# Kernel optimization log

Hardware: AMD Instinct MI355X
Metric: run time of the kernel (lower is better)

Reference implementation:

```python
import jax, jax.numpy as jnp
import numpy as np

BN_EPS = 1e-5

def _conv(x, w, pad):
    return jax.lax.conv_general_dilated(
        x, w, window_strides=(1, 1), padding=[(pad, pad), (pad, pad)],
        dimension_numbers=('NCHW', 'OIHW', 'NCHW'))

def setup_inputs() -> dict:
    key = jax.random.key(0)
    ks = jax.random.split(key, 6)
    B, C1, C2, H, W, k = 4, 128, 256, 64, 64, 3
    N = k * k
    x = jax.random.normal(ks[0], (B, C1, H, W), jnp.float32)
    pw_w = jax.random.normal(ks[1], (C2, C1, 1, 1), jnp.float32) * 0.05
    bn_gamma = jnp.ones((C2,), jnp.float32)
    bn_beta = jnp.zeros((C2,), jnp.float32)
    bn_mean = jax.random.normal(ks[2], (C2,), jnp.float32) * 0.1
    bn_var = jax.random.uniform(ks[3], (C2,), jnp.float32, minval=0.5, maxval=1.5)
    off_w = jax.random.normal(ks[4], (2 * N, C2, 3, 3), jnp.float32) * 0.01
    off_b = jnp.zeros((2 * N,), jnp.float32)
    dcn_w = jax.random.normal(ks[5], (C2, C2, k, k), jnp.float32) * 0.02
    return dict(x=x, pw_w=pw_w, bn_gamma=bn_gamma, bn_beta=bn_beta,
                bn_mean=bn_mean, bn_var=bn_var, off_w=off_w, off_b=off_b,
                dcn_w=dcn_w)

def reference(x, pw_w, bn_gamma, bn_beta, bn_mean, bn_var, off_w, off_b, dcn_w):
    B, C1, H, W = x.shape
    C2 = pw_w.shape[0]
    k = dcn_w.shape[-1]
    N = k * k
    # ---- 1x1 pointwise conv + BatchNorm (eval mode), act=False ----
    xp = _conv(x, pw_w, 0)
    scale = bn_gamma * jax.lax.rsqrt(bn_var + BN_EPS)
    xp = xp * scale[None, :, None, None] + (bn_beta - bn_mean * scale)[None, :, None, None]
    # ---- offset prediction conv: [B, 2N, H, W]; first N = dy, last N = dx ----
    offset = _conv(xp, off_w, 1) + off_b[None, :, None, None]
    off_y, off_x = offset[:, :N], offset[:, N:]
    # ---- sampling positions p = p0 + p_n + offset ----
    gy, gx = jnp.meshgrid(jnp.arange(H, dtype=jnp.float32),
                          jnp.arange(W, dtype=jnp.float32), indexing='ij')
    kk = jnp.arange(k, dtype=jnp.float32) - (k // 2)
    ky, kx = jnp.meshgrid(kk, kk, indexing='ij')
    py = gy[None, None] + ky.reshape(N)[None, :, None, None] + off_y  # [B,N,H,W]
    px = gx[None, None] + kx.reshape(N)[None, :, None, None] + off_x
    py = jnp.clip(py, 0.0, H - 1.0)
    px = jnp.clip(px, 0.0, W - 1.0)

    def sample_one(img, py_b, px_b):  # img [C2,H,W], py/px [N,H,W]
        y0 = jnp.floor(py_b)
        x0 = jnp.floor(px_b)
        wy = py_b - y0
        wx = px_b - x0
        y0i = y0.astype(jnp.int32)
        x0i = x0.astype(jnp.int32)
        y1i = jnp.minimum(y0i + 1, H - 1)
        x1i = jnp.minimum(x0i + 1, W - 1)
        flat = img.reshape(C2, H * W)
        def g(yy, xx):
            idx = (yy * W + xx).reshape(-1)
            return flat[:, idx].reshape(C2, N, H, W)
        v00 = g(y0i, x0i); v01 = g(y0i, x1i)
        v10 = g(y1i, x0i); v11 = g(y1i, x1i)
        wy = wy[None]; wx = wx[None]
        return (v00 * (1 - wy) * (1 - wx) + v01 * (1 - wy) * wx +
                v10 * wy * (1 - wx) + v11 * wy * wx)

    sampled = jax.vmap(sample_one)(xp, py, px)  # [B,C2,N,H,W]
    # ---- deformable conv = weighted sum over kernel points ----
    out = jnp.einsum('bcnhw,ocn->bohw', sampled, dcn_w.reshape(C2, C2, N))
    return jax.nn.silu(out)
```

## Files before the change

kernel.cpp:

```cpp
#include <hip/hip_runtime.h>
#include <math.h>

#define XP_F   0
#define OFF_F  4194304
#define XPH_F  4489216
#define WTB_F  6586368
#define PART_F 6881280
#define SAMP_F 9240576
#define SPLIT_END_F 28114944ULL

typedef short bf16x8 __attribute__((ext_vector_type(8)));
typedef float f32x4 __attribute__((ext_vector_type(4)));

__device__ inline unsigned short f2b(float f) {
    union { float f; unsigned u; } v; v.f = f;
    unsigned r = v.u + 0x7FFF + ((v.u >> 16) & 1);
    return (unsigned short)(r >> 16);
}
__device__ inline float b2f(unsigned short h) {
    union { unsigned u; float f; } v; v.u = ((unsigned)h) << 16; return v.f;
}

__global__ __launch_bounds__(256) void k0_prep(const float* __restrict__ dcn,
                                               unsigned short* __restrict__ wTb) {
    int idx = blockIdx.x * 256 + threadIdx.x;
    int n = idx >> 16, o = (idx >> 8) & 255, c = idx & 255;
    wTb[idx] = f2b(dcn[(o * 256 + c) * 9 + n]);
}

__global__ __launch_bounds__(256, 4) void k1_pw_bn(const float* __restrict__ x,
                                                   const float* __restrict__ pw,
                                                   const float* __restrict__ gamma,
                                                   const float* __restrict__ beta,
                                                   const float* __restrict__ mean,
                                                   const float* __restrict__ var,
                                                   float* __restrict__ xp,
                                                   unsigned short* __restrict__ xph) {
    __shared__ float wl[128 * 64];
    int t = threadIdx.x;
    int m0 = blockIdx.x * 64;
    int b = m0 >> 12;
    int hw = (m0 & 4095) + (t & 63);
    int q = t >> 6;
    int c2base = blockIdx.y * 64;

    for (int i = 0; i < 32; ++i) {
        int idx = t + 256 * i;
        int kk = idx >> 6, c2l = idx & 63;
        wl[idx] = pw[(c2base + c2l) * 128 + kk];
    }
    __syncthreads();

    float acc[16];
#pragma unroll
    for (int i = 0; i < 16; ++i) acc[i] = 0.f;

    const float* xb = x + (b * 128) * 4096 + hw;
    for (int kk = 0; kk < 128; kk += 8) {
        float xv[8];
#pragma unroll
        for (int u = 0; u < 8; ++u) xv[u] = xb[(kk + u) * 4096];
#pragma unroll
        for (int u = 0; u < 8; ++u) {
            const float4* w4 = (const float4*)&wl[(kk + u) * 64 + q * 16];
#pragma unroll
            for (int i = 0; i < 4; ++i) {
                float4 wv = w4[i];
                acc[i * 4 + 0] += xv[u] * wv.x;
                acc[i * 4 + 1] += xv[u] * wv.y;
                acc[i * 4 + 2] += xv[u] * wv.z;
                acc[i * 4 + 3] += xv[u] * wv.w;
            }
        }
    }
    bf16x8 r0, r1;
#pragma unroll
    for (int i = 0; i < 16; ++i) {
        int c2 = c2base + q * 16 + i;
        float s = gamma[c2] * rsqrtf(var[c2] + 1e-5f);
        float v = acc[i] * s + (beta[c2] - mean[c2] * s);
        xp[((b * 256 + c2) << 12) + hw] = v;
        if (i < 8) r0[i] = (short)f2b(v); else r1[i - 8] = (short)f2b(v);
    }
    unsigned short* hb = xph + (((b << 12) + hw) << 8) + c2base + q * 16;
    *(bf16x8*)hb = r0;
    *(bf16x8*)(hb + 8) = r1;
}

__global__ __launch_bounds__(256) void k2a_off(const float* __restrict__ xp,
                                               const float* __restrict__ offw,
                                               float* __restrict__ part) {
    __shared__ float xl[3 * 32 * 66];
    __shared__ float wl[9 * 18 * 32];
    int t = threadIdx.x;
    int bx = blockIdx.x;
    int b = bx >> 9, h = (bx >> 3) & 63, cs = bx & 7;
    int w = t & 63, jset = t >> 6;
    const int jbase_a[4] = {0, 5, 10, 14};
    const int jcnt_a[4] = {5, 5, 4, 4};
    int jbase = jbase_a[jset], jcnt = jcnt_a[jset];
    float acc[5] = {0.f, 0.f, 0.f, 0.f, 0.f};
    int cbase = cs * 32;

    for (int idx = t; idx < 3 * 32 * 66; idx += 256) {
        int dy = idx / 2112, rem = idx % 2112;
        int c = rem / 66, col = rem % 66;
        int y = h + dy - 1, wc = col - 1;
        float v = 0.f;
        if ((unsigned)y < 64u && (unsigned)wc < 64u)
            v = xp[((b * 256 + cbase + c) << 12) + y * 64 + wc];
        xl[idx] = v;
    }
    for (int idx = t; idx < 18 * 32 * 9; idx += 256) {
        int j = idx / 288, c = (idx / 9) % 32, tap = idx % 9;
        wl[(tap * 18 + j) * 32 + c] = offw[(j * 256 + cbase + c) * 9 + tap];
    }
    __syncthreads();
#pragma unroll
    for (int tap = 0; tap < 9; ++tap) {
        int dy = tap / 3, dx = tap % 3;
        const float* xrow = &xl[dy * 2112 + (w + dx)];
        const float4* wrow = (const float4*)&wl[(tap * 18 + jbase) * 32];
#pragma unroll
        for (int c4 = 0; c4 < 8; ++c4) {
            float xv0 = xrow[(c4 * 4 + 0) * 66];
            float xv1 = xrow[(c4 * 4 + 1) * 66];
            float xv2 = xrow[(c4 * 4 + 2) * 66];
            float xv3 = xrow[(c4 * 4 + 3) * 66];
#pragma unroll
            for (int jj = 0; jj < 5; ++jj) {
                if (jj < jcnt) {
                    float4 wv = wrow[jj * 8 + c4];
                    acc[jj] += xv0 * wv.x + xv1 * wv.y + xv2 * wv.z + xv3 * wv.w;
                }
            }
        }
    }
    for (int jj = 0; jj < 5; ++jj) {
        if (jj < jcnt)
            part[(((cs * 4 + b) * 18 + jbase + jj) << 12) + h * 64 + w] = acc[jj];
    }
}

__global__ __launch_bounds__(256) void k2b_red(const float* __restrict__ part,
                                               const float* __restrict__ offb,
                                               float* __restrict__ off) {
    int i = blockIdx.x * 256 + threadIdx.x;
    int j = (i >> 12) % 18;
    float s = offb[j];
#pragma unroll
    for (int cs = 0; cs < 8; ++cs) s += part[cs * 294912 + i];
    off[i] = s;
}

__global__ __launch_bounds__(256) void k3a_samp(const unsigned short* __restrict__ xph,
                                                const float* __restrict__ off,
                                                unsigned short* __restrict__ samp) {
    __shared__ int   c00[32], c01[32], c10[32], c11[32];
    __shared__ float4 wts[32];
    int t = threadIdx.x;
    int bid = blockIdx.x;
    int b = bid / 1152, r = bid % 1152;
    int tap = r >> 7, pb = r & 127;
    int h = pb >> 1, wh = (pb & 1) * 32;

    if (t < 32) {
        int w = wh + t;
        int hw = h * 64 + w;
        float oy = off[((b * 18 + tap) << 12) + hw];
        float ox = off[((b * 18 + tap + 9) << 12) + hw];
        float py = (float)(h + tap / 3 - 1) + oy;
        float px = (float)(w + tap % 3 - 1) + ox;
        py = fminf(fmaxf(py, 0.f), 63.f);
        px = fminf(fmaxf(px, 0.f), 63.f);
        float fy = floorf(py), fx = floorf(px);
        int y0 = (int)fy, x0 = (int)fx;
        float wy = py - fy, wx = px - fx;
        int y1 = min(y0 + 1, 63), x1 = min(x0 + 1, 63);
        c00[t] = (y0 * 64 + x0) << 8;  c01[t] = (y0 * 64 + x1) << 8;
        c10[t] = (y1 * 64 + x0) << 8;  c11[t] = (y1 * 64 + x1) << 8;
        wts[t] = make_float4((1.f - wy) * (1.f - wx), (1.f - wy) * wx,
                             wy * (1.f - wx), wy * wx);
    }
    __syncthreads();

    const unsigned short* xb = xph + (b << 20);
    unsigned short* sb = samp + bid * 8192;
#pragma unroll
    for (int i = 0; i < 4; ++i) {
        int u = i * 256 + t;
        int F = u >> 6, chunk = u & 63;
        int lane = chunk ^ (F & 7);
        int pxl = (F >> 3) * 16 + (lane & 15);
        int co = ((F & 7) * 4 + (lane >> 4)) << 3;
        float4 wv = wts[pxl];
        bf16x8 v00 = *(const bf16x8*)(xb + c00[pxl] + co);
        bf16x8 v01 = *(const bf16x8*)(xb + c01[pxl] + co);
        bf16x8 v10 = *(const bf16x8*)(xb + c10[pxl] + co);
        bf16x8 v11 = *(const bf16x8*)(xb + c11[pxl] + co);
        bf16x8 rr;
#pragma unroll
        for (int j = 0; j < 8; ++j) {
            float v = wv.x * b2f((unsigned short)v00[j]) +
                      wv.y * b2f((unsigned short)v01[j]) +
                      wv.z * b2f((unsigned short)v10[j]) +
                      wv.w * b2f((unsigned short)v11[j]);
            rr[j] = (short)f2b(v);
        }
        *(bf16x8*)(sb + (u << 3)) = rr;
    }
}

__global__ __launch_bounds__(512, 4) void k3b_gemm(const unsigned short* __restrict__ samp,
                                                   const unsigned short* __restrict__ wTb,
                                                   float* __restrict__ out) {
    __shared__ unsigned short smp[2][8192];
    int t = threadIdx.x;
    int orig = blockIdx.x;
    int bx = (orig & 7) * 64 + (orig >> 3);
    int b = bx >> 7, h = (bx >> 1) & 63, half = bx & 1, wh = half * 32;
    int wv = t >> 6, l = t & 63;
    int tile0 = (b * 9) * 128 + h * 2 + half;

    auto stage = [&](int tap) {
        const unsigned short* src = samp + (tile0 + tap * 128) * 8192 + t * 8;
        unsigned short* dst = &smp[tap & 1][t * 8];
#if __has_builtin(__builtin_amdgcn_global_load_lds)
        __builtin_amdgcn_global_load_lds(
            (const __attribute__((address_space(1))) unsigned int*)src,
            (__attribute__((address_space(3))) unsigned int*)dst, 16, 0, 0);
        __builtin_amdgcn_global_load_lds(
            (const __attribute__((address_space(1))) unsigned int*)(src + 4096),
            (__attribute__((address_space(3))) unsigned int*)(dst + 4096), 16, 0, 0);
#else
        *(bf16x8*)dst = *(const bf16x8*)src;
        *(bf16x8*)(dst + 4096) = *(const bf16x8*)(src + 4096);
#endif
    };

    stage(0);
    __syncthreads();

    f32x4 acc[2][2];
#pragma unroll
    for (int i = 0; i < 2; ++i)
#pragma unroll
        for (int j = 0; j < 2; ++j) acc[i][j] = (f32x4)0.f;

    int arow = l & 15, areg = l >> 4;
    for (int tap = 0; tap < 9; ++tap) {
        if (tap < 8) stage(tap + 1);
        int bu = tap & 1;
        const unsigned short* wbase =
            wTb + (tap * 256 + wv * 32 + arow) * 256 + areg * 8;
        __builtin_amdgcn_s_setprio(1);
#pragma unroll
        for (int ks = 0; ks < 8; ++ks) {
            bf16x8 a0 = *(const bf16x8*)(wbase + ks * 32);
            bf16x8 a1 = *(const bf16x8*)(wbase + 16 * 256 + ks * 32);
#pragma unroll
            for (int pt = 0; pt < 2; ++pt) {
                int F = pt * 8 + ks;
                bf16x8 bfr = *(const bf16x8*)
                    &smp[bu][(F * 64 + (l ^ (F & 7))) << 3];
                acc[0][pt] = __builtin_amdgcn_mfma_f32_16x16x32_bf16(a0, bfr, acc[0][pt], 0, 0, 0);
                acc[1][pt] = __builtin_amdgcn_mfma_f32_16x16x32_bf16(a1, bfr, acc[1][pt], 0, 0, 0);
            }
        }
        __builtin_amdgcn_s_setprio(0);
        __syncthreads();
    }

#pragma unroll
    for (int ot = 0; ot < 2; ++ot)
#pragma unroll
        for (int pt = 0; pt < 2; ++pt) {
            int px = wh + pt * 16 + (l & 15);
#pragma unroll
            for (int j = 0; j < 4; ++j) {
                int o = wv * 32 + ot * 16 + (l >> 4) * 4 + j;
                float a = acc[ot][pt][j];
                out[((b * 256 + o) << 12) + h * 64 + px] = a / (1.f + expf(-a));
            }
        }
}

__global__ __launch_bounds__(512, 4) void k3_dcn(const unsigned short* __restrict__ xph,
                                                 const float* __restrict__ off,
                                                 const unsigned short* __restrict__ wTb,
                                                 float* __restrict__ out) {
    __shared__ int   i00[288], i01[288], i10[288], i11[288];
    __shared__ float w00[288], w01[288], w10[288], w11[288];
    __shared__ unsigned short smp[2][16 * 64 * 8];
    int t = threadIdx.x;
    int orig = blockIdx.x;
    int bx = (orig & 7) * 64 + (orig >> 3);
    int b = bx >> 7, h = (bx >> 1) & 63, wh = (bx & 1) * 32;
    int wv = t >> 6, l = t & 63;
    const unsigned short* xb = xph + (b << 20);

    if (t < 288) {
        int n = t >> 5, p = t & 31;
        int w = wh + p;
        float oy = off[((b * 18 + n) << 12) + h * 64 + w];
        float ox = off[((b * 18 + n + 9) << 12) + h * 64 + w];
        float py = (float)(h + n / 3 - 1) + oy;
        float px = (float)(w + n % 3 - 1) + ox;
        py = fminf(fmaxf(py, 0.f), 63.f);
        px = fminf(fmaxf(px, 0.f), 63.f);
        float fy = floorf(py), fx = floorf(px);
        int y0 = (int)fy, x0 = (int)fx;
        float wy = py - fy, wx = px - fx;
        int y1 = min(y0 + 1, 63), x1 = min(x0 + 1, 63);
        i00[t] = (y0 * 64 + x0) << 8;  i01[t] = (y0 * 64 + x1) << 8;
        i10[t] = (y1 * 64 + x0) << 8;  i11[t] = (y1 * 64 + x1) << 8;
        w00[t] = (1.f - wy) * (1.f - wx);  w01[t] = (1.f - wy) * wx;
        w10[t] = wy * (1.f - wx);          w11[t] = wy * wx;
    }
    __syncthreads();

    int pt_p = wv & 1;
    int ks0 = wv >> 1;
    int px_p = pt_p * 16 + (l & 15);
    int cgl = l >> 4;
    bf16x8 g[2][4];

    auto stage_issue = [&](int tap) {
        int sb = tap * 32 + px_p;
        int a00 = i00[sb], a01 = i01[sb], a10 = i10[sb], a11 = i11[sb];
#pragma unroll
        for (int ku = 0; ku < 2; ++ku) {
            int ks = ks0 + ku * 4;
            int c = (ks * 4 + cgl) << 3;
            g[ku][0] = *(const bf16x8*)(xb + a00 + c);
            g[ku][1] = *(const bf16x8*)(xb + a01 + c);
            g[ku][2] = *(const bf16x8*)(xb + a10 + c);
            g[ku][3] = *(const bf16x8*)(xb + a11 + c);
        }
    };
    auto stage_write = [&](int tap) {
        int bu = tap & 1;
        int sb = tap * 32 + px_p;
        float b00 = w00[sb], b01 = w01[sb], b10 = w10[sb], b11 = w11[sb];
#pragma unroll
        for (int ku = 0; ku < 2; ++ku) {
            bf16x8 r;
#pragma unroll
            for (int j = 0; j < 8; ++j) {
                float v = b00 * b2f((unsigned short)g[ku][0][j]) +
                          b01 * b2f((unsigned short)g[ku][1][j]) +
                          b10 * b2f((unsigned short)g[ku][2][j]) +
                          b11 * b2f((unsigned short)g[ku][3][j]);
                r[j] = (short)f2b(v);
            }
            int F = pt_p * 8 + ks0 + ku * 4;
            *(bf16x8*)&smp[bu][(F * 64 + (l ^ (F & 7))) << 3] = r;
        }
    };

    stage_issue(0);
    __builtin_amdgcn_sched_barrier(0);
    stage_write(0);
    __syncthreads();

    f32x4 acc[2][2];
#pragma unroll
    for (int i = 0; i < 2; ++i)
#pragma unroll
        for (int j = 0; j < 2; ++j) acc[i][j] = (f32x4)0.f;

    int arow = l & 15, areg = l >> 4;
    for (int tap = 0; tap < 9; ++tap) {
        if (tap < 8) stage_issue(tap + 1);
        __builtin_amdgcn_sched_barrier(0);
        int bu = tap & 1;
        const unsigned short* wbase =
            wTb + (tap * 256 + wv * 32 + arow) * 256 + areg * 8;
        __builtin_amdgcn_s_setprio(1);
#pragma unroll
        for (int ks = 0; ks < 8; ++ks) {
            bf16x8 a0 = *(const bf16x8*)(wbase + ks * 32);
            bf16x8 a1 = *(const bf16x8*)(wbase + 16 * 256 + ks * 32);
#pragma unroll
            for (int pt = 0; pt < 2; ++pt) {
                int F = pt * 8 + ks;
                bf16x8 bfr = *(const bf16x8*)
                    &smp[bu][(F * 64 + (l ^ (F & 7))) << 3];
                acc[0][pt] = __builtin_amdgcn_mfma_f32_16x16x32_bf16(a0, bfr, acc[0][pt], 0, 0, 0);
                acc[1][pt] = __builtin_amdgcn_mfma_f32_16x16x32_bf16(a1, bfr, acc[1][pt], 0, 0, 0);
            }
        }
        __builtin_amdgcn_s_setprio(0);
        __builtin_amdgcn_sched_barrier(0);
        if (tap < 8) stage_write(tap + 1);
        __syncthreads();
    }

#pragma unroll
    for (int ot = 0; ot < 2; ++ot)
#pragma unroll
        for (int pt = 0; pt < 2; ++pt) {
            int px = wh + pt * 16 + (l & 15);
#pragma unroll
            for (int j = 0; j < 4; ++j) {
                int o = wv * 32 + ot * 16 + (l >> 4) * 4 + j;
                float a = acc[ot][pt][j];
                out[((b * 256 + o) << 12) + h * 64 + px] = a / (1.f + expf(-a));
            }
        }
}

extern "C" void kernel_launch(void* const* d_in, const int* in_sizes, int n_in,
                              void* d_out, int out_size, void* d_ws, size_t ws_size,
                              hipStream_t stream) {
    const float* x     = (const float*)d_in[0];
    const float* pw    = (const float*)d_in[1];
    const float* gamma = (const float*)d_in[2];
    const float* beta  = (const float*)d_in[3];
    const float* mean  = (const float*)d_in[4];
    const float* var   = (const float*)d_in[5];
    const float* offw  = (const float*)d_in[6];
    const float* offb  = (const float*)d_in[7];
    const float* dcn   = (const float*)d_in[8];
    float* ws = (float*)d_ws;
    float* xp   = ws + XP_F;
    float* off  = ws + OFF_F;
    unsigned short* xph = (unsigned short*)(ws + XPH_F);
    unsigned short* wTb = (unsigned short*)(ws + WTB_F);
    float* part = ws + PART_F;
    unsigned short* samp = (unsigned short*)(ws + SAMP_F);
    float* out = (float*)d_out;

    hipLaunchKernelGGL(k0_prep, dim3(2304), dim3(256), 0, stream, dcn, wTb);
    hipLaunchKernelGGL(k1_pw_bn, dim3(256, 4), dim3(256), 0, stream,
                       x, pw, gamma, beta, mean, var, xp, xph);
    hipLaunchKernelGGL(k2a_off, dim3(2048), dim3(256), 0, stream, xp, offw, part);
    hipLaunchKernelGGL(k2b_red, dim3(1152), dim3(256), 0, stream, part, offb, off);
    if (ws_size >= SPLIT_END_F * 4ULL) {
        hipLaunchKernelGGL(k3a_samp, dim3(4608), dim3(256), 0, stream, xph, off, samp);
        hipLaunchKernelGGL(k3b_gemm, dim3(512), dim3(512), 0, stream, samp, wTb, out);
    } else {
        hipLaunchKernelGGL(k3_dcn, dim3(512), dim3(512), 0, stream, xph, off, wTb, out);
    }
}
```

Baseline: 289.3 us.

## Stage GEMM weights through swizzled LDS and enlarge tile to full row

```diff
diff --git a/kernel.cpp b/kernel.cpp
--- a/kernel.cpp
+++ b/kernel.cpp
@@ -211,34 +211,55 @@
     }
 }
 
-__global__ __launch_bounds__(512, 4) void k3b_gemm(const unsigned short* __restrict__ samp,
-                                                   const unsigned short* __restrict__ wTb,
-                                                   float* __restrict__ out) {
-    __shared__ unsigned short smp[2][8192];
+__global__ __launch_bounds__(1024, 4) void k3b_gemm(const unsigned short* __restrict__ samp,
+                                                    const unsigned short* __restrict__ wTb,
+                                                    float* __restrict__ out) {
+    __shared__ unsigned short ldsA[2][16384];
+    __shared__ unsigned short ldsB[2][16384];
     int t = threadIdx.x;
     int orig = blockIdx.x;
-    int bx = (orig & 7) * 64 + (orig >> 3);
-    int b = bx >> 7, h = (bx >> 1) & 63, half = bx & 1, wh = half * 32;
+    int bx = (orig & 7) * 32 + (orig >> 3);
+    int b = bx >> 6, hh = bx & 63;
     int wv = t >> 6, l = t & 63;
-    int tile0 = (b * 9) * 128 + h * 2 + half;
-
-    auto stage = [&](int tap) {
-        const unsigned short* src = samp + (tile0 + tap * 128) * 8192 + t * 8;
-        unsigned short* dst = &smp[tap & 1][t * 8];
+    int ow = wv >> 1, pxh = wv & 1;
+    int tile0 = (b * 9) * 128 + hh * 2;
+
+    auto stageA = [&](int tap, int ksub, int buf) {
+        const unsigned short* base = wTb + tap * 65536 + ksub * 64;
+#pragma unroll
+        for (int k = 0; k < 2; ++k) {
+            int u = t + k * 1024;
+            int r = u >> 3, c = u & 7;
+            const unsigned short* src = base + r * 256 + ((c ^ (r & 7)) << 3);
+            unsigned short* dst = &ldsA[buf][u << 3];
 #if __has_builtin(__builtin_amdgcn_global_load_lds)
-        __builtin_amdgcn_global_load_lds(
-            (const __attribute__((address_space(1))) unsigned int*)src,
-            (__attribute__((address_space(3))) unsigned int*)dst, 16, 0, 0);
-        __builtin_amdgcn_global_load_lds(
-            (const __attribute__((address_space(1))) unsigned int*)(src + 4096),
-            (__attribute__((address_space(3))) unsigned int*)(dst + 4096), 16, 0, 0);
+            __builtin_amdgcn_global_load_lds(
+                (const __attribute__((address_space(1))) unsigned int*)src,
+                (__attribute__((address_space(3))) unsigned int*)dst, 16, 0, 0);
 #else
-        *(bf16x8*)dst = *(const bf16x8*)src;
-        *(bf16x8*)(dst + 4096) = *(const bf16x8*)(src + 4096);
+            *(bf16x8*)dst = *(const bf16x8*)src;
 #endif
+        }
     };
-
-    stage(0);
+    auto stageB = [&](int tap, int buf) {
+        const unsigned short* sb = samp + (size_t)(tile0 + tap * 128) * 8192;
+#pragma unroll
+        for (int k = 0; k < 2; ++k) {
+            int u = t + k * 1024;
+            const unsigned short* src = sb + (u << 3);
+            unsigned short* dst = &ldsB[buf][u << 3];
+#if __has_builtin(__builtin_amdgcn_global_load_lds)
+            __builtin_amdgcn_global_load_lds(
+                (const __attribute__((address_space(1))) unsigned int*)src,
+                (__attribute__((address_space(3))) unsigned int*)dst, 16, 0, 0);
+#else
+            *(bf16x8*)dst = *(const bf16x8*)src;
+#endif
+        }
+    };
+
+    stageA(0, 0, 0);
+    stageB(0, 0);
     __syncthreads();
 
     f32x4 acc[2][2];
@@ -247,40 +268,49 @@
 #pragma unroll
         for (int j = 0; j < 2; ++j) acc[i][j] = (f32x4)0.f;
 
-    int arow = l & 15, areg = l >> 4;
+    int bufA = 0, bufB = 0;
     for (int tap = 0; tap < 9; ++tap) {
-        if (tap < 8) stage(tap + 1);
-        int bu = tap & 1;
-        const unsigned short* wbase =
-            wTb + (tap * 256 + wv * 32 + arow) * 256 + areg * 8;
-        __builtin_amdgcn_s_setprio(1);
-#pragma unroll
-        for (int ks = 0; ks < 8; ++ks) {
-            bf16x8 a0 = *(const bf16x8*)(wbase + ks * 32);
-            bf16x8 a1 = *(const bf16x8*)(wbase + 16 * 256 + ks * 32);
-#pragma unroll
-            for (int pt = 0; pt < 2; ++pt) {
-                int F = pt * 8 + ks;
-                bf16x8 bfr = *(const bf16x8*)
-                    &smp[bu][(F * 64 + (l ^ (F & 7))) << 3];
-                acc[0][pt] = __builtin_amdgcn_mfma_f32_16x16x32_bf16(a0, bfr, acc[0][pt], 0, 0, 0);
-                acc[1][pt] = __builtin_amdgcn_mfma_f32_16x16x32_bf16(a1, bfr, acc[1][pt], 0, 0, 0);
-            }
-        }
-        __builtin_amdgcn_s_setprio(0);
-        __syncthreads();
+#pragma unroll
+        for (int ksub = 0; ksub < 4; ++ksub) {
+            if (ksub < 3) stageA(tap, ksub + 1, bufA ^ 1);
+            else if (tap < 8) stageA(tap + 1, 0, bufA ^ 1);
+            if (ksub == 0 && tap < 8) stageB(tap + 1, bufB ^ 1);
+
+            __builtin_amdgcn_s_setprio(1);
+#pragma unroll
+            for (int ks2 = 0; ks2 < 2; ++ks2) {
+#pragma unroll
+                for (int ot = 0; ot < 2; ++ot) {
+                    int r = ow * 32 + ot * 16 + (l & 15);
+                    bf16x8 a = *(const bf16x8*)
+                        &ldsA[bufA][(r << 6) + (((((l >> 4) + (ks2 << 2))) ^ (r & 7)) << 3)];
+#pragma unroll
+                    for (int pt = 0; pt < 2; ++pt) {
+                        int F = pt * 8 + ksub * 2 + ks2;
+                        bf16x8 bb = *(const bf16x8*)
+                            &ldsB[bufB][(pxh << 13) + ((F * 64 + (l ^ (F & 7))) << 3)];
+                        acc[ot][pt] = __builtin_amdgcn_mfma_f32_16x16x32_bf16(
+                            a, bb, acc[ot][pt], 0, 0, 0);
+                    }
+                }
+            }
+            __builtin_amdgcn_s_setprio(0);
+            __syncthreads();
+            bufA ^= 1;
+        }
+        bufB ^= 1;
     }
 
 #pragma unroll
     for (int ot = 0; ot < 2; ++ot)
 #pragma unroll
         for (int pt = 0; pt < 2; ++pt) {
-            int px = wh + pt * 16 + (l & 15);
+            int px = pxh * 32 + pt * 16 + (l & 15);
 #pragma unroll
             for (int j = 0; j < 4; ++j) {
-                int o = wv * 32 + ot * 16 + (l >> 4) * 4 + j;
+                int o = ow * 32 + ot * 16 + (l >> 4) * 4 + j;
                 float a = acc[ot][pt][j];
-                out[((b * 256 + o) << 12) + h * 64 + px] = a / (1.f + expf(-a));
+                out[((b * 256 + o) << 12) + hh * 64 + px] = a / (1.f + expf(-a));
             }
         }
 }
@@ -438,7 +468,7 @@
     hipLaunchKernelGGL(k2b_red, dim3(1152), dim3(256), 0, stream, part, offb, off);
     if (ws_size >= SPLIT_END_F * 4ULL) {
         hipLaunchKernelGGL(k3a_samp, dim3(4608), dim3(256), 0, stream, xph, off, samp);
-        hipLaunchKernelGGL(k3b_gemm, dim3(512), dim3(512), 0, stream, samp, wTb, out);
+        hipLaunchKernelGGL(k3b_gemm, dim3(256), dim3(1024), 0, stream, samp, wTb, out);
     } else {
         hipLaunchKernelGGL(k3_dcn, dim3(512), dim3(512), 0, stream, xph, off, wTb, out);
     }
```

Result: faster. 252.7 us (-12.7%).
